# Optimization experiments

Hardware: AMD Instinct MI355X
Metric: run time of the kernel (lower is better)

The kernel has to match this reference:

```python
import jax, jax.numpy as jnp
import numpy as np
from jax.scipy.special import gammaln

BIG_NEG = -1e9
MAX_K = 20  # args.sm_max_span_length


def setup_inputs() -> dict:
    key = jax.random.key(0)
    ks = jax.random.split(key, 7)
    B, N, d, C = 16, 2048, 256, 128
    features = jax.random.normal(ks[0], (B, N, d), dtype=jnp.float32)
    lengths = jax.random.randint(ks[1], (B,), N // 2, N + 1)
    gaussian_means = jax.random.normal(ks[2], (C, d), dtype=jnp.float32)
    cov_diag = jax.random.uniform(ks[3], (d,), minval=0.5, maxval=1.5, dtype=jnp.float32)
    transition_logits = jax.random.normal(ks[4], (C, C), dtype=jnp.float32)
    init_logits = jax.random.uniform(ks[5], (C,), dtype=jnp.float32)
    poisson_log_rates = jax.random.normal(ks[6], (C,), dtype=jnp.float32) * 0.5 + 1.5
    return {"features": features, "lengths": lengths, "gaussian_means": gaussian_means,
            "cov_diag": cov_diag, "transition_logits": transition_logits,
            "init_logits": init_logits, "poisson_log_rates": poisson_log_rates}


def _emission_log_probs(features, means, cov_diag):
    # Diagonal-covariance MultivariateNormal log-prob, one class per column.
    # Quadratic form expanded to avoid materializing [B,N,C,d].
    inv_var = 1.0 / cov_diag
    d = features.shape[-1]
    const = -0.5 * (d * jnp.log(2.0 * jnp.pi) + jnp.sum(jnp.log(cov_diag)))
    xq = jnp.einsum('bnd,d->bn', features * features, inv_var)          # [B,N]
    mq = jnp.einsum('cd,d->c', means * means, inv_var)                  # [C]
    xm = jnp.einsum('bnd,cd->bnc', features, means * inv_var)           # [B,N,C]
    return const - 0.5 * (xq[..., None] + mq[None, None, :] - 2.0 * xm)  # [B,N,C]


def _length_log_probs(log_rates, K):
    # Poisson log-prob for span lengths k = 1..K.
    ks = jnp.arange(1, K + 1, dtype=jnp.float32)[:, None]               # [K,1]
    return ks * log_rates[None, :] - jnp.exp(log_rates)[None, :] - gammaln(ks + 1.0)  # [K,C]


def _transition_log_probs(transition_logits):
    C = transition_logits.shape[0]
    masked = jnp.where(jnp.eye(C, dtype=bool), BIG_NEG, transition_logits)  # no self-transitions
    return jax.nn.log_softmax(masked, axis=0)  # normalized over destination class (dim 0)


def _semimarkov_logZ(emis_lp, lengths, init_lp, trans_lp, len_lp, K):
    # Segmental (semi-Markov) CRF forward algorithm with sliding-window span sums.
    B, N, C = emis_lp.shape
    cum = jnp.concatenate([jnp.zeros((B, 1, C), emis_lp.dtype), jnp.cumsum(emis_lp, axis=1)], axis=1)
    cum_pad = jnp.concatenate([jnp.zeros((B, K, C), emis_lp.dtype), cum], axis=1)  # idx t+K <-> position t
    beta0 = jnp.full((B, N + 1 + K, C), BIG_NEG, emis_lp.dtype)
    beta0 = beta0.at[:, K, :].set(init_lp[None, :])  # position 0: initial distribution
    len_rev = len_lp[::-1]  # len_rev[j] == length log-prob of span length K-j

    def step(beta, t):
        w = jax.lax.dynamic_slice(beta, (0, t, 0), (B, K, C))        # beta at positions t-K..t-1
        cw = jax.lax.dynamic_slice(cum_pad, (0, t, 0), (B, K, C))
        ct = jax.lax.dynamic_slice(cum_pad, (0, t + K, 0), (B, 1, C))
        span = w + len_rev[None, :, :] + (ct - cw)                    # [B,K,C] span scores ending at t
        alpha_t = jax.nn.logsumexp(span, axis=1)                      # [B,C]
        beta_t = jax.nn.logsumexp(alpha_t[:, None, :] + trans_lp[None, :, :], axis=2)  # to-class
        beta = jax.lax.dynamic_update_slice(beta, beta_t[:, None, :], (0, t + K, 0))
        return beta, alpha_t

    _, alphas = jax.lax.scan(step, beta0, jnp.arange(1, N + 1))       # alphas: [N,B,C]
    final = alphas[lengths - 1, jnp.arange(B)]                        # [B,C] at each sequence end
    return jax.nn.logsumexp(final, axis=1)                            # [B] log partition


def reference(features, lengths, gaussian_means, cov_diag, transition_logits, init_logits, poisson_log_rates):
    emis_lp = _emission_log_probs(features, gaussian_means, cov_diag)
    init_lp = jax.nn.log_softmax(init_logits, axis=0)
    trans_lp = _transition_log_probs(transition_logits)
    len_lp = _length_log_probs(poisson_log_rates, MAX_K)
    return _semimarkov_logZ(emis_lp, lengths, init_lp, trans_lp, len_lp, MAX_K)
```

## Files before the change

kernel.cpp:

```cpp
#include <hip/hip_runtime.h>
#include <math.h>

#define Bb 16
#define Nn 2048
#define Dd 256
#define Cc 128
#define Kk 20
#define BIG_NEG -1.0e9f
#define LOG2E 1.4426950408889634f
#define LN2   0.6931471805599453f

#define WS_EMIS   0
#define WS_MSC    (WS_EMIS + Bb*Nn*Cc)
#define WS_XQ     (WS_MSC + Cc*Dd)
#define WS_ECHAN  (WS_XQ + Bb*Nn)
#define WS_T      (WS_ECHAN + Cc)
#define WS_LEN    (WS_T + Cc*Cc)
#define WS_INIT   (WS_LEN + Kk*Cc)
#define WS_IVAR   (WS_INIT + Cc)

typedef __attribute__((ext_vector_type(8))) short short8;
typedef __attribute__((ext_vector_type(4))) float float4v;
typedef __attribute__((ext_vector_type(8))) int int8v;

__device__ __forceinline__ unsigned short f32_to_bf16(float x) {
  unsigned int u = __builtin_bit_cast(unsigned int, x);
  u = (u + 0x7FFFu + ((u >> 16) & 1u)) >> 16;
  return (unsigned short)u;
}

#define DPP_STEP(x, op, ctrl, rmask)                                          \
  do {                                                                        \
    int _yi = __builtin_amdgcn_update_dpp(                                    \
        __builtin_bit_cast(int, x), __builtin_bit_cast(int, x), ctrl, rmask,  \
        0xF, true);                                                           \
    x = op(x, __builtin_bit_cast(float, _yi));                                \
  } while (0)

__device__ __forceinline__ float dpp_add(float a, float b) { return a + b; }

__device__ __forceinline__ float wave_max64(float x) {
  DPP_STEP(x, fmaxf, 0xB1, 0xF);
  DPP_STEP(x, fmaxf, 0x4E, 0xF);
  DPP_STEP(x, fmaxf, 0x141, 0xF);
  DPP_STEP(x, fmaxf, 0x140, 0xF);
  DPP_STEP(x, fmaxf, 0x142, 0xA);
  DPP_STEP(x, fmaxf, 0x143, 0xC);
  return __builtin_bit_cast(float,
      __builtin_amdgcn_readlane(__builtin_bit_cast(int, x), 63));
}

__device__ __forceinline__ float wave_sum64(float x) {
  DPP_STEP(x, dpp_add, 0xB1, 0xF);
  DPP_STEP(x, dpp_add, 0x4E, 0xF);
  DPP_STEP(x, dpp_add, 0x141, 0xF);
  DPP_STEP(x, dpp_add, 0x140, 0xF);
  DPP_STEP(x, dpp_add, 0x142, 0xA);
  DPP_STEP(x, dpp_add, 0x143, 0xC);
  return __builtin_bit_cast(float,
      __builtin_amdgcn_readlane(__builtin_bit_cast(int, x), 63));
}

__device__ __forceinline__ int chan_of_k(int kpos) {
  return (kpos & 1) ? (64 + (kpos >> 1)) : (kpos >> 1);
}

__global__ void prep_kernel(const float* __restrict__ means,
                            const float* __restrict__ cov,
                            const float* __restrict__ tl,
                            const float* __restrict__ il,
                            const float* __restrict__ plr,
                            float* __restrict__ ws) {
  __shared__ float s_iv[Dd];
  __shared__ float s_red[4];
  __shared__ float s_tlse[Cc];
  int tid = threadIdx.x;

  float cv = cov[tid];
  float iv = 1.0f / cv;
  s_iv[tid] = iv;
  ws[WS_IVAR + tid] = iv;
  float lg = __logf(cv);
  #pragma unroll
  for (int off = 1; off < 64; off <<= 1) lg += __shfl_xor(lg, off, 64);
  if ((tid & 63) == 0) s_red[tid >> 6] = lg;
  __syncthreads();
  float logdet = s_red[0] + s_red[1] + s_red[2] + s_red[3];
  float cconst = -0.5f * ((float)Dd * 1.8378770664093453f + logdet);

  unsigned short* mscb = (unsigned short*)(ws + WS_MSC);
  for (int idx = tid; idx < Cc * Dd; idx += 256) {
    int d = idx & (Dd - 1);
    mscb[idx] = f32_to_bf16(means[idx] * s_iv[d]);
  }
  if (tid < Cc) {
    float acc = 0.0f;
    for (int d = 0; d < Dd; d++) {
      float m = means[tid * Dd + d];
      acc = fmaf(m * m, s_iv[d], acc);
    }
    ws[WS_ECHAN + tid] = cconst - 0.5f * acc;
  }
  for (int idx = tid; idx < Kk * Cc; idx += 256) {
    int L = idx / Cc + 1;
    int c = idx & (Cc - 1);
    float r = plr[c];
    ws[WS_LEN + idx] = ((float)L * r - __expf(r) - lgammaf((float)(L + 1))) * LOG2E;
  }

  __syncthreads();
  float x = (tid < Cc) ? il[tid] : -INFINITY;
  float mx = x;
  #pragma unroll
  for (int off = 1; off < 64; off <<= 1) mx = fmaxf(mx, __shfl_xor(mx, off, 64));
  if ((tid & 63) == 0) s_red[tid >> 6] = mx;
  __syncthreads();
  float M = fmaxf(s_red[0], s_red[1]);
  float se = (tid < Cc) ? __expf(x - M) : 0.0f;
  #pragma unroll
  for (int off = 1; off < 64; off <<= 1) se += __shfl_xor(se, off, 64);
  __syncthreads();
  if ((tid & 63) == 0) s_red[tid >> 6] = se;
  __syncthreads();
  float lse = M + __logf(s_red[0] + s_red[1]);
  if (tid < Cc) ws[WS_INIT + tid] = (x - lse) * LOG2E;

  if (tid < Cc) {
    int j = tid;
    float m2 = -INFINITY;
    for (int i = 0; i < Cc; i++) if (i != j) m2 = fmaxf(m2, tl[i * Cc + j]);
    float s2 = 0.0f;
    for (int i = 0; i < Cc; i++) if (i != j) s2 += __expf(tl[i * Cc + j] - m2);
    s_tlse[j] = m2 + __logf(s2);
  }
  __syncthreads();
  for (int idx = tid; idx < Cc * Cc; idx += 256) {
    int i = idx / Cc;
    int j = idx & (Cc - 1);
    ws[WS_T + idx] = (i == j) ? 0.0f : __expf(tl[idx] - s_tlse[j]);
  }
}

__global__ void xq_kernel(const float* __restrict__ f, float* __restrict__ ws) {
  int pos = blockIdx.x * 4 + (threadIdx.x >> 6);
  int lane = threadIdx.x & 63;
  const float4 fv = *(const float4*)&f[(size_t)pos * Dd + lane * 4];
  const float4 vv = *(const float4*)&ws[WS_IVAR + lane * 4];
  float a = fv.x * fv.x * vv.x + fv.y * fv.y * vv.y +
            fv.z * fv.z * vv.z + fv.w * fv.w * vv.w;
  #pragma unroll
  for (int off = 1; off < 64; off <<= 1) a += __shfl_xor(a, off, 64);
  if (lane == 0) ws[WS_XQ + pos] = a;
}

__launch_bounds__(256)
__global__ void emis_mfma_kernel(const float* __restrict__ f, float* __restrict__ ws) {
  const unsigned short* msc = (const unsigned short*)(ws + WS_MSC);
  float* emis = ws + WS_EMIS;
  int tid = threadIdx.x;
  int w = tid >> 6, lane = tid & 63, g = lane >> 4, l16 = lane & 15;
  int b = blockIdx.x >> 6;
  int n0 = (blockIdx.x & 63) << 5;
  int c0 = w << 5;

  const float* fbase = f + (size_t)(b * Nn + n0) * Dd;
  float4v acc[2][2];
  #pragma unroll
  for (int rt = 0; rt < 2; rt++)
    #pragma unroll
    for (int ct = 0; ct < 2; ct++) acc[rt][ct] = (float4v){0.f, 0.f, 0.f, 0.f};

  #pragma unroll
  for (int k0 = 0; k0 < Dd; k0 += 32) {
    int kk = k0 + g * 8;
    short8 afr[2], bfr[2];
    #pragma unroll
    for (int rt = 0; rt < 2; rt++) {
      const float* src = fbase + (size_t)(rt * 16 + l16) * Dd + kk;
      float4 v0 = *(const float4*)src;
      float4 v1 = *(const float4*)(src + 4);
      short8 fr;
      fr[0] = (short)f32_to_bf16(v0.x); fr[1] = (short)f32_to_bf16(v0.y);
      fr[2] = (short)f32_to_bf16(v0.z); fr[3] = (short)f32_to_bf16(v0.w);
      fr[4] = (short)f32_to_bf16(v1.x); fr[5] = (short)f32_to_bf16(v1.y);
      fr[6] = (short)f32_to_bf16(v1.z); fr[7] = (short)f32_to_bf16(v1.w);
      afr[rt] = fr;
    }
    #pragma unroll
    for (int ct = 0; ct < 2; ct++)
      bfr[ct] = *(const short8*)&msc[(size_t)(c0 + ct * 16 + l16) * Dd + kk];
    #pragma unroll
    for (int rt = 0; rt < 2; rt++)
      #pragma unroll
      for (int ct = 0; ct < 2; ct++)
        acc[rt][ct] = __builtin_amdgcn_mfma_f32_16x16x32_bf16(afr[rt], bfr[ct], acc[rt][ct], 0, 0, 0);
  }

  #pragma unroll
  for (int rt = 0; rt < 2; rt++) {
    #pragma unroll
    for (int ct = 0; ct < 2; ct++) {
      int cc = c0 + ct * 16 + l16;
      float ec = ws[WS_ECHAN + cc];
      #pragma unroll
      for (int r = 0; r < 4; r++) {
        int row = rt * 16 + g * 4 + r;
        int nn = n0 + row;
        emis[(size_t)(b * Nn + nn) * Cc + cc] =
            (ec - 0.5f * ws[WS_XQ + b * Nn + nn] + acc[rt][ct][r]) * LOG2E;
      }
    }
  }
}

__launch_bounds__(64, 1)
__global__ void scan_kernel(const int* __restrict__ lengths,
                            const float* __restrict__ ws,
                            float* __restrict__ out) {
  __shared__ unsigned short s_p[64];
  int lane = threadIdx.x;
  int lg4 = lane >> 4, n16 = lane & 15;
  int b = blockIdx.x;
  int len_b = lengths[b];
  const float* emis = ws + WS_EMIS + (size_t)b * Nn * Cc;
  const int sc1 = 0x7F7F7F7F;

  int8v Tf[8];
  {
    const float* T = ws + WS_T;
    #pragma unroll
    for (int nt = 0; nt < 8; nt++) {
      const float* Trow = &T[(size_t)(nt * 16 + n16) * Cc];
      #pragma unroll
      for (int dw = 0; dw < 8; dw++) {
        int kbase = lg4 * 32 + dw * 4;
        float t0 = 64.0f * Trow[chan_of_k(kbase + 0)];
        float t1 = 64.0f * Trow[chan_of_k(kbase + 1)];
        float t2 = 64.0f * Trow[chan_of_k(kbase + 2)];
        float t3 = 64.0f * Trow[chan_of_k(kbase + 3)];
        int d = __builtin_amdgcn_cvt_pk_fp8_f32(t0, t1, 0, false);
        d = __builtin_amdgcn_cvt_pk_fp8_f32(t2, t3, d, true);
        Tf[nt][dw] = d;
      }
    }
  }

  int cidx[2] = {lane, lane + 64};
  float len0[2], E2[2][Kk - 1];
  #pragma unroll
  for (int ch = 0; ch < 2; ch++) {
    float lenv[Kk];
    #pragma unroll
    for (int k = 0; k < Kk; k++) lenv[k] = ws[WS_LEN + k * Cc + cidx[ch]];
    len0[ch] = lenv[0];
    #pragma unroll
    for (int k = 0; k < Kk - 1; k++)
      E2[ch][k] = __builtin_amdgcn_exp2f(lenv[k + 1] - lenv[k]);
  }

  float wv[2][Kk - 1];
  #pragma unroll
  for (int ch = 0; ch < 2; ch++)
    #pragma unroll
    for (int j = 0; j < Kk - 1; j++) wv[ch][j] = 0.0f;
  float a[2] = {0.0f, 0.0f};
  float L19[2] = {-1.0e30f, -1.0e30f};
  float gnew[2], cum[2];
  gnew[0] = ws[WS_INIT + lane];
  gnew[1] = ws[WS_INIT + lane + 64];
  cum[0] = emis[0 * Cc + lane];
  cum[1] = emis[0 * Cc + lane + 64];

  float e[2][8], en[2][8];
  #pragma unroll
  for (int i = 0; i < 8; i++) {
    e[0][i] = emis[(size_t)(1 + i) * Cc + lane];
    e[1][i] = emis[(size_t)(1 + i) * Cc + lane + 64];
  }

  bool done = false;
  for (int tg = 1; tg <= Nn && !done; tg += 8) {
    #pragma unroll
    for (int i = 0; i < 8; i++) {
      int t = tg + i;
      {
        int r = tg + 8 + i; if (r > Nn - 1) r = Nn - 1;
        en[0][i] = emis[(size_t)r * Cc + lane];
        en[1][i] = emis[(size_t)r * Cc + lane + 64];
      }

      float h0[2], mm[2], eh[2], sfix[2], mab[2];
      #pragma unroll
      for (int ch = 0; ch < 2; ch++) {
        h0[ch] = gnew[ch] + len0[ch];
        mm[ch] = fmaxf(L19[ch], h0[ch]);
        float eL = __builtin_amdgcn_exp2f(L19[ch] - mm[ch]);
        eh[ch] = __builtin_amdgcn_exp2f(h0[ch] - mm[ch]);
        sfix[ch] = eL + eh[ch];
        mab[ch] = mm[ch] + cum[ch];
      }
      float lmax = fmaxf(mab[0], mab[1]);
      float wm = wave_max64(lmax);
      float p0 = sfix[0] * __builtin_amdgcn_exp2f(mab[0] - wm);
      float p1 = sfix[1] * __builtin_amdgcn_exp2f(mab[1] - wm);
      int pk = __builtin_amdgcn_cvt_pk_fp8_f32(p0, p1, 0, false);
      s_p[lane] = (unsigned short)pk;
      bool is_out = (t == len_b);

      const int4* ap = (const int4*)((const char*)s_p + lg4 * 32);
      int4 ra = ap[0];
      int4 rb = ap[1];
      int8v A;
      A[0] = ra.x; A[1] = ra.y; A[2] = ra.z; A[3] = ra.w;
      A[4] = rb.x; A[5] = rb.y; A[6] = rb.z; A[7] = rb.w;

      float4v D0, D1, D2, D3, D4, D5, D6, D7;
      {
        float4v z = {0.0f, 0.0f, 0.0f, 0.0f};
        D0 = __builtin_amdgcn_mfma_scale_f32_16x16x128_f8f6f4(A, Tf[0], z, 0, 0, 0, sc1, 0, sc1);
        D1 = __builtin_amdgcn_mfma_scale_f32_16x16x128_f8f6f4(A, Tf[1], z, 0, 0, 0, sc1, 0, sc1);
        D2 = __builtin_amdgcn_mfma_scale_f32_16x16x128_f8f6f4(A, Tf[2], z, 0, 0, 0, sc1, 0, sc1);
        D3 = __builtin_amdgcn_mfma_scale_f32_16x16x128_f8f6f4(A, Tf[3], z, 0, 0, 0, sc1, 0, sc1);
        D4 = __builtin_amdgcn_mfma_scale_f32_16x16x128_f8f6f4(A, Tf[4], z, 0, 0, 0, sc1, 0, sc1);
        D5 = __builtin_amdgcn_mfma_scale_f32_16x16x128_f8f6f4(A, Tf[5], z, 0, 0, 0, sc1, 0, sc1);
        D6 = __builtin_amdgcn_mfma_scale_f32_16x16x128_f8f6f4(A, Tf[6], z, 0, 0, 0, sc1, 0, sc1);
        D7 = __builtin_amdgcn_mfma_scale_f32_16x16x128_f8f6f4(A, Tf[7], z, 0, 0, 0, sc1, 0, sc1);
      }

      float S19n[2];
      #pragma unroll
      for (int ch = 0; ch < 2; ch++) {
        float phi = __builtin_amdgcn_exp2f(a[ch] - mm[ch]);
        #pragma unroll
        for (int j = Kk - 2; j >= 1; j--)
          wv[ch][j] = wv[ch][j - 1] * (E2[ch][j] * phi);
        wv[ch][0] = eh[ch] * E2[ch][0];
        float s4[5];
        s4[0] = (wv[ch][0] + wv[ch][1]) + (wv[ch][2] + wv[ch][3]);
        s4[1] = (wv[ch][4] + wv[ch][5]) + (wv[ch][6] + wv[ch][7]);
        s4[2] = (wv[ch][8] + wv[ch][9]) + (wv[ch][10] + wv[ch][11]);
        s4[3] = (wv[ch][12] + wv[ch][13]) + (wv[ch][14] + wv[ch][15]);
        s4[4] = (wv[ch][16] + wv[ch][17]) + wv[ch][18];
        S19n[ch] = ((s4[0] + s4[1]) + (s4[2] + s4[3])) + s4[4];
      }

      float q0 = (lg4 == 0) ? D0[0] : (lg4 == 1) ? D1[0] : (lg4 == 2) ? D2[0] : D3[0];
      float q1 = (lg4 == 0) ? D4[0] : (lg4 == 1) ? D5[0] : (lg4 == 2) ? D6[0] : D7[0];
      float rel0 = cum[0] - wm;
      float rel1 = cum[1] - wm;
      gnew[0] = (q0 > 0.0f) ? (__builtin_amdgcn_logf(q0) - 6.0f - rel0) : BIG_NEG;
      gnew[1] = (q1 > 0.0f) ? (__builtin_amdgcn_logf(q1) - 6.0f - rel1) : BIG_NEG;

      if (is_out) {
        float psum = wave_sum64(p0 + p1);
        if (lane == 0) out[b] = LN2 * (wm + __builtin_amdgcn_logf(psum));
        done = true;
        break;
      }

      #pragma unroll
      for (int ch = 0; ch < 2; ch++) {
        a[ch] = mm[ch];
        L19[ch] = mm[ch] + __builtin_amdgcn_logf(S19n[ch]);
        cum[ch] += e[ch][i];
      }
    }
    if (!done) {
      #pragma unroll
      for (int i = 0; i < 8; i++) { e[0][i] = en[0][i]; e[1][i] = en[1][i]; }
    }
  }
}

extern "C" void kernel_launch(void* const* d_in, const int* in_sizes, int n_in,
                              void* d_out, int out_size, void* d_ws, size_t ws_size,
                              hipStream_t stream) {
  const float* features = (const float*)d_in[0];
  const int* lengths = (const int*)d_in[1];
  const float* means = (const float*)d_in[2];
  const float* cov = (const float*)d_in[3];
  const float* tl = (const float*)d_in[4];
  const float* il = (const float*)d_in[5];
  const float* plr = (const float*)d_in[6];
  float* out = (float*)d_out;
  float* ws = (float*)d_ws;

  prep_kernel<<<1, 256, 0, stream>>>(means, cov, tl, il, plr, ws);
  xq_kernel<<<(Bb * Nn) / 4, 256, 0, stream>>>(features, ws);
  emis_mfma_kernel<<<Bb * (Nn / 32), 256, 0, stream>>>(features, ws);
  scan_kernel<<<Bb, 64, 0, stream>>>(lengths, ws, out);
}
```

Measured before the change: 1.551 ms.

## Interleave two batch sequences per scan wave and parallelize prep mean reduction

Each scan wave now advances two independent batch sequences in lockstep, so one sequence's dependent chain (wave reductions, LDS round trip, MFMA, exp/log) can hide the latency of the other. The scan launches half as many blocks and runs until the longer of the two lengths. The per-class mean quadratic term in the prep kernel is now split across two threads with vectorized loads and combined through shared memory. The costs are roughly double the register pressure in the scan, possible spills, some wasted steps when paired lengths differ, and an added clamp on phi to keep the finished sequence's values bounded.

```diff
diff --git a/kernel.cpp b/kernel.cpp
--- a/kernel.cpp
+++ b/kernel.cpp
@@ -74,6 +74,7 @@
   __shared__ float s_iv[Dd];
   __shared__ float s_red[4];
   __shared__ float s_tlse[Cc];
+  __shared__ float s_mq[256];
   int tid = threadIdx.x;
 
   float cv = cov[tid];
@@ -93,13 +94,21 @@
     int d = idx & (Dd - 1);
     mscb[idx] = f32_to_bf16(means[idx] * s_iv[d]);
   }
-  if (tid < Cc) {
+  {
+    int c = tid >> 1, half = tid & 1;
     float acc = 0.0f;
-    for (int d = 0; d < Dd; d++) {
-      float m = means[tid * Dd + d];
-      acc = fmaf(m * m, s_iv[d], acc);
-    }
-    ws[WS_ECHAN + tid] = cconst - 0.5f * acc;
+    const float* mrow = means + (size_t)c * Dd + half * 128;
+    const float* ivp = s_iv + half * 128;
+    #pragma unroll
+    for (int d = 0; d < 128; d += 4) {
+      float4 mv = *(const float4*)&mrow[d];
+      float4 vv = *(const float4*)&ivp[d];
+      acc = fmaf(mv.x * mv.x, vv.x, acc);
+      acc = fmaf(mv.y * mv.y, vv.y, acc);
+      acc = fmaf(mv.z * mv.z, vv.z, acc);
+      acc = fmaf(mv.w * mv.w, vv.w, acc);
+    }
+    s_mq[tid] = acc;
   }
   for (int idx = tid; idx < Kk * Cc; idx += 256) {
     int L = idx / Cc + 1;
@@ -109,6 +118,9 @@
   }
 
   __syncthreads();
+  if (tid < Cc)
+    ws[WS_ECHAN + tid] = cconst - 0.5f * (s_mq[2 * tid] + s_mq[2 * tid + 1]);
+
   float x = (tid < Cc) ? il[tid] : -INFINITY;
   float mx = x;
   #pragma unroll
@@ -217,12 +229,17 @@
 __global__ void scan_kernel(const int* __restrict__ lengths,
                             const float* __restrict__ ws,
                             float* __restrict__ out) {
-  __shared__ unsigned short s_p[64];
+  __shared__ unsigned short s_p[2][64];
   int lane = threadIdx.x;
   int lg4 = lane >> 4, n16 = lane & 15;
-  int b = blockIdx.x;
-  int len_b = lengths[b];
-  const float* emis = ws + WS_EMIS + (size_t)b * Nn * Cc;
+  int bA = blockIdx.x, bB = blockIdx.x + 8;
+  int lenA = lengths[bA], lenB = lengths[bB];
+  int tmax = max(lenA, lenB);
+  const float* emisP[2];
+  emisP[0] = ws + WS_EMIS + (size_t)bA * Nn * Cc;
+  emisP[1] = ws + WS_EMIS + (size_t)bB * Nn * Cc;
+  int lenP[2] = {lenA, lenB};
+  int outP[2] = {bA, bB};
   const int sc1 = 0x7F7F7F7F;
 
   int8v Tf[8];
@@ -258,24 +275,23 @@
       E2[ch][k] = __builtin_amdgcn_exp2f(lenv[k + 1] - lenv[k]);
   }
 
-  float wv[2][Kk - 1];
-  #pragma unroll
-  for (int ch = 0; ch < 2; ch++)
-    #pragma unroll
-    for (int j = 0; j < Kk - 1; j++) wv[ch][j] = 0.0f;
-  float a[2] = {0.0f, 0.0f};
-  float L19[2] = {-1.0e30f, -1.0e30f};
-  float gnew[2], cum[2];
-  gnew[0] = ws[WS_INIT + lane];
-  gnew[1] = ws[WS_INIT + lane + 64];
-  cum[0] = emis[0 * Cc + lane];
-  cum[1] = emis[0 * Cc + lane + 64];
-
-  float e[2][8], en[2][8];
-  #pragma unroll
-  for (int i = 0; i < 8; i++) {
-    e[0][i] = emis[(size_t)(1 + i) * Cc + lane];
-    e[1][i] = emis[(size_t)(1 + i) * Cc + lane + 64];
+  float wv[2][2][Kk - 1];
+  float aa[2][2], L19[2][2], gnew[2][2], cum[2][2];
+  float e[2][2][8], en[2][2][8];
+  #pragma unroll
+  for (int bi = 0; bi < 2; bi++) {
+    #pragma unroll
+    for (int ch = 0; ch < 2; ch++) {
+      #pragma unroll
+      for (int j = 0; j < Kk - 1; j++) wv[bi][ch][j] = 0.0f;
+      aa[bi][ch] = 0.0f;
+      L19[bi][ch] = -1.0e30f;
+      gnew[bi][ch] = ws[WS_INIT + cidx[ch]];
+      cum[bi][ch] = emisP[bi][0 * Cc + cidx[ch]];
+      #pragma unroll
+      for (int i = 0; i < 8; i++)
+        e[bi][ch][i] = emisP[bi][(size_t)(1 + i) * Cc + cidx[ch]];
+    }
   }
 
   bool done = false;
@@ -283,91 +299,94 @@
     #pragma unroll
     for (int i = 0; i < 8; i++) {
       int t = tg + i;
-      {
-        int r = tg + 8 + i; if (r > Nn - 1) r = Nn - 1;
-        en[0][i] = emis[(size_t)r * Cc + lane];
-        en[1][i] = emis[(size_t)r * Cc + lane + 64];
+      #pragma unroll
+      for (int bi = 0; bi < 2; bi++) {
+        {
+          int r = tg + 8 + i; if (r > Nn - 1) r = Nn - 1;
+          en[bi][0][i] = emisP[bi][(size_t)r * Cc + lane];
+          en[bi][1][i] = emisP[bi][(size_t)r * Cc + lane + 64];
+        }
+
+        float h0[2], mm[2], eh[2], sfix[2], mab[2];
+        #pragma unroll
+        for (int ch = 0; ch < 2; ch++) {
+          h0[ch] = gnew[bi][ch] + len0[ch];
+          mm[ch] = fmaxf(L19[bi][ch], h0[ch]);
+          float eL = __builtin_amdgcn_exp2f(L19[bi][ch] - mm[ch]);
+          eh[ch] = __builtin_amdgcn_exp2f(h0[ch] - mm[ch]);
+          sfix[ch] = eL + eh[ch];
+          mab[ch] = mm[ch] + cum[bi][ch];
+        }
+        float lmax = fmaxf(mab[0], mab[1]);
+        float wm = wave_max64(lmax);
+        float p0 = sfix[0] * __builtin_amdgcn_exp2f(mab[0] - wm);
+        float p1 = sfix[1] * __builtin_amdgcn_exp2f(mab[1] - wm);
+        int pk = __builtin_amdgcn_cvt_pk_fp8_f32(p0, p1, 0, false);
+        s_p[bi][lane] = (unsigned short)pk;
+        bool is_out = (t == lenP[bi]);
+        if (is_out) {
+          float psum = wave_sum64(p0 + p1);
+          if (lane == 0) out[outP[bi]] = LN2 * (wm + __builtin_amdgcn_logf(psum));
+        }
+
+        const int4* ap = (const int4*)((const char*)s_p[bi] + lg4 * 32);
+        int4 ra = ap[0];
+        int4 rb = ap[1];
+        int8v A;
+        A[0] = ra.x; A[1] = ra.y; A[2] = ra.z; A[3] = ra.w;
+        A[4] = rb.x; A[5] = rb.y; A[6] = rb.z; A[7] = rb.w;
+
+        float S19n[2];
+        #pragma unroll
+        for (int ch = 0; ch < 2; ch++) {
+          float phi = __builtin_amdgcn_exp2f(fminf(aa[bi][ch] - mm[ch], 100.0f));
+          #pragma unroll
+          for (int j = Kk - 2; j >= 1; j--)
+            wv[bi][ch][j] = wv[bi][ch][j - 1] * (E2[ch][j] * phi);
+          wv[bi][ch][0] = eh[ch] * E2[ch][0];
+          float s4[5];
+          s4[0] = (wv[bi][ch][0] + wv[bi][ch][1]) + (wv[bi][ch][2] + wv[bi][ch][3]);
+          s4[1] = (wv[bi][ch][4] + wv[bi][ch][5]) + (wv[bi][ch][6] + wv[bi][ch][7]);
+          s4[2] = (wv[bi][ch][8] + wv[bi][ch][9]) + (wv[bi][ch][10] + wv[bi][ch][11]);
+          s4[3] = (wv[bi][ch][12] + wv[bi][ch][13]) + (wv[bi][ch][14] + wv[bi][ch][15]);
+          s4[4] = (wv[bi][ch][16] + wv[bi][ch][17]) + wv[bi][ch][18];
+          S19n[ch] = ((s4[0] + s4[1]) + (s4[2] + s4[3])) + s4[4];
+        }
+
+        float4v D0, D1, D2, D3, D4, D5, D6, D7;
+        {
+          float4v z = {0.0f, 0.0f, 0.0f, 0.0f};
+          D0 = __builtin_amdgcn_mfma_scale_f32_16x16x128_f8f6f4(A, Tf[0], z, 0, 0, 0, sc1, 0, sc1);
+          D1 = __builtin_amdgcn_mfma_scale_f32_16x16x128_f8f6f4(A, Tf[1], z, 0, 0, 0, sc1, 0, sc1);
+          D2 = __builtin_amdgcn_mfma_scale_f32_16x16x128_f8f6f4(A, Tf[2], z, 0, 0, 0, sc1, 0, sc1);
+          D3 = __builtin_amdgcn_mfma_scale_f32_16x16x128_f8f6f4(A, Tf[3], z, 0, 0, 0, sc1, 0, sc1);
+          D4 = __builtin_amdgcn_mfma_scale_f32_16x16x128_f8f6f4(A, Tf[4], z, 0, 0, 0, sc1, 0, sc1);
+          D5 = __builtin_amdgcn_mfma_scale_f32_16x16x128_f8f6f4(A, Tf[5], z, 0, 0, 0, sc1, 0, sc1);
+          D6 = __builtin_amdgcn_mfma_scale_f32_16x16x128_f8f6f4(A, Tf[6], z, 0, 0, 0, sc1, 0, sc1);
+          D7 = __builtin_amdgcn_mfma_scale_f32_16x16x128_f8f6f4(A, Tf[7], z, 0, 0, 0, sc1, 0, sc1);
+        }
+        float q0 = (lg4 == 0) ? D0[0] : (lg4 == 1) ? D1[0] : (lg4 == 2) ? D2[0] : D3[0];
+        float q1 = (lg4 == 0) ? D4[0] : (lg4 == 1) ? D5[0] : (lg4 == 2) ? D6[0] : D7[0];
+        float rel0 = cum[bi][0] - wm;
+        float rel1 = cum[bi][1] - wm;
+        gnew[bi][0] = (q0 > 0.0f) ? (__builtin_amdgcn_logf(q0) - 6.0f - rel0) : BIG_NEG;
+        gnew[bi][1] = (q1 > 0.0f) ? (__builtin_amdgcn_logf(q1) - 6.0f - rel1) : BIG_NEG;
+
+        #pragma unroll
+        for (int ch = 0; ch < 2; ch++) {
+          aa[bi][ch] = mm[ch];
+          L19[bi][ch] = mm[ch] + __builtin_amdgcn_logf(S19n[ch]);
+          cum[bi][ch] += e[bi][ch][i];
+        }
       }
-
-      float h0[2], mm[2], eh[2], sfix[2], mab[2];
-      #pragma unroll
-      for (int ch = 0; ch < 2; ch++) {
-        h0[ch] = gnew[ch] + len0[ch];
-        mm[ch] = fmaxf(L19[ch], h0[ch]);
-        float eL = __builtin_amdgcn_exp2f(L19[ch] - mm[ch]);
-        eh[ch] = __builtin_amdgcn_exp2f(h0[ch] - mm[ch]);
-        sfix[ch] = eL + eh[ch];
-        mab[ch] = mm[ch] + cum[ch];
+      if (t == tmax) { done = true; break; }
+    }
+    if (!done) {
+      #pragma unroll
+      for (int i = 0; i < 8; i++) {
+        e[0][0][i] = en[0][0][i]; e[0][1][i] = en[0][1][i];
+        e[1][0][i] = en[1][0][i]; e[1][1][i] = en[1][1][i];
       }
-      float lmax = fmaxf(mab[0], mab[1]);
-      float wm = wave_max64(lmax);
-      float p0 = sfix[0] * __builtin_amdgcn_exp2f(mab[0] - wm);
-      float p1 = sfix[1] * __builtin_amdgcn_exp2f(mab[1] - wm);
-      int pk = __builtin_amdgcn_cvt_pk_fp8_f32(p0, p1, 0, false);
-      s_p[lane] = (unsigned short)pk;
-      bool is_out = (t == len_b);
-
-      const int4* ap = (const int4*)((const char*)s_p + lg4 * 32);
-      int4 ra = ap[0];
-      int4 rb = ap[1];
-      int8v A;
-      A[0] = ra.x; A[1] = ra.y; A[2] = ra.z; A[3] = ra.w;
-      A[4] = rb.x; A[5] = rb.y; A[6] = rb.z; A[7] = rb.w;
-
-      float4v D0, D1, D2, D3, D4, D5, D6, D7;
-      {
-        float4v z = {0.0f, 0.0f, 0.0f, 0.0f};
-        D0 = __builtin_amdgcn_mfma_scale_f32_16x16x128_f8f6f4(A, Tf[0], z, 0, 0, 0, sc1, 0, sc1);
-        D1 = __builtin_amdgcn_mfma_scale_f32_16x16x128_f8f6f4(A, Tf[1], z, 0, 0, 0, sc1, 0, sc1);
-        D2 = __builtin_amdgcn_mfma_scale_f32_16x16x128_f8f6f4(A, Tf[2], z, 0, 0, 0, sc1, 0, sc1);
-        D3 = __builtin_amdgcn_mfma_scale_f32_16x16x128_f8f6f4(A, Tf[3], z, 0, 0, 0, sc1, 0, sc1);
-        D4 = __builtin_amdgcn_mfma_scale_f32_16x16x128_f8f6f4(A, Tf[4], z, 0, 0, 0, sc1, 0, sc1);
-        D5 = __builtin_amdgcn_mfma_scale_f32_16x16x128_f8f6f4(A, Tf[5], z, 0, 0, 0, sc1, 0, sc1);
-        D6 = __builtin_amdgcn_mfma_scale_f32_16x16x128_f8f6f4(A, Tf[6], z, 0, 0, 0, sc1, 0, sc1);
-        D7 = __builtin_amdgcn_mfma_scale_f32_16x16x128_f8f6f4(A, Tf[7], z, 0, 0, 0, sc1, 0, sc1);
-      }
-
-      float S19n[2];
-      #pragma unroll
-      for (int ch = 0; ch < 2; ch++) {
-        float phi = __builtin_amdgcn_exp2f(a[ch] - mm[ch]);
-        #pragma unroll
-        for (int j = Kk - 2; j >= 1; j--)
-          wv[ch][j] = wv[ch][j - 1] * (E2[ch][j] * phi);
-        wv[ch][0] = eh[ch] * E2[ch][0];
-        float s4[5];
-        s4[0] = (wv[ch][0] + wv[ch][1]) + (wv[ch][2] + wv[ch][3]);
-        s4[1] = (wv[ch][4] + wv[ch][5]) + (wv[ch][6] + wv[ch][7]);
-        s4[2] = (wv[ch][8] + wv[ch][9]) + (wv[ch][10] + wv[ch][11]);
-        s4[3] = (wv[ch][12] + wv[ch][13]) + (wv[ch][14] + wv[ch][15]);
-        s4[4] = (wv[ch][16] + wv[ch][17]) + wv[ch][18];
-        S19n[ch] = ((s4[0] + s4[1]) + (s4[2] + s4[3])) + s4[4];
-      }
-
-      float q0 = (lg4 == 0) ? D0[0] : (lg4 == 1) ? D1[0] : (lg4 == 2) ? D2[0] : D3[0];
-      float q1 = (lg4 == 0) ? D4[0] : (lg4 == 1) ? D5[0] : (lg4 == 2) ? D6[0] : D7[0];
-      float rel0 = cum[0] - wm;
-      float rel1 = cum[1] - wm;
-      gnew[0] = (q0 > 0.0f) ? (__builtin_amdgcn_logf(q0) - 6.0f - rel0) : BIG_NEG;
-      gnew[1] = (q1 > 0.0f) ? (__builtin_amdgcn_logf(q1) - 6.0f - rel1) : BIG_NEG;
-
-      if (is_out) {
-        float psum = wave_sum64(p0 + p1);
-        if (lane == 0) out[b] = LN2 * (wm + __builtin_amdgcn_logf(psum));
-        done = true;
-        break;
-      }
-
-      #pragma unroll
-      for (int ch = 0; ch < 2; ch++) {
-        a[ch] = mm[ch];
-        L19[ch] = mm[ch] + __builtin_amdgcn_logf(S19n[ch]);
-        cum[ch] += e[ch][i];
-      }
-    }
-    if (!done) {
-      #pragma unroll
-      for (int i = 0; i < 8; i++) { e[0][i] = en[0][i]; e[1][i] = en[1][i]; }
     }
   }
 }
@@ -388,5 +407,5 @@
   prep_kernel<<<1, 256, 0, stream>>>(means, cov, tl, il, plr, ws);
   xq_kernel<<<(Bb * Nn) / 4, 256, 0, stream>>>(features, ws);
   emis_mfma_kernel<<<Bb * (Nn / 32), 256, 0, stream>>>(features, ws);
-  scan_kernel<<<Bb, 64, 0, stream>>>(lengths, ws, out);
-}
+  scan_kernel<<<8, 64, 0, stream>>>(lengths, ws, out);
+}
```

New measurement: 3.006 ms. +93.8%, slower.
